# Kernel optimization log

Hardware: AMD Instinct MI355X
Metric: run time of the kernel (lower is better)

Reference implementation:

```python
import jax, jax.numpy as jnp
import numpy as np
import math

B, S, I, C = 1, 256, 512, 256   # batch, msa rows, residues, c_s
H, D = 8, 32                     # num_heads, head_dim; total = H*D = 256
EPS = 1e-5


def setup_inputs() -> dict:
    key = jax.random.key(0)
    ks = jax.random.split(key, 10)
    s = 0.02
    return {
        "msa_representation": jax.random.normal(ks[0], (B, S, I, C), jnp.float32),
        "ln_gamma": jnp.ones((C,), jnp.float32),
        "ln_beta": jnp.zeros((C,), jnp.float32),
        # weights stored [in, out] (torch Linear applies x @ W.T; equivalent math)
        "Wq": jax.random.normal(ks[1], (C, H * D), jnp.float32) * s,
        "Wk": jax.random.normal(ks[2], (C, D), jnp.float32) * s,
        "Wv": jax.random.normal(ks[3], (C, D), jnp.float32) * s,
        "Wg": jax.random.normal(ks[4], (C, H * D), jnp.float32) * s,
        "bg": jnp.zeros((H * D,), jnp.float32),
        "Wo": jax.random.normal(ks[5], (H * D, C), jnp.float32) * s,
        "bo": jnp.zeros((C,), jnp.float32),
    }


def reference(msa_representation, ln_gamma, ln_beta, Wq, Wk, Wv, Wg, bg, Wo, bo):
    x = msa_representation
    mu = jnp.mean(x, axis=-1, keepdims=True)
    var = jnp.mean(jnp.square(x - mu), axis=-1, keepdims=True)
    x = (x - mu) * jax.lax.rsqrt(var + EPS) * ln_gamma + ln_beta  # [B,S,I,C]

    Q = (x @ Wq).reshape(B, S, I, H, D).mean(axis=1)              # [B,I,H,D]
    K = x @ Wk                                                    # [B,S,I,D] ('btid')
    V = x @ Wv                                                    # [B,S,I,D]
    G = jax.nn.sigmoid(x @ Wg + bg).reshape(B, S, I, H, D)        # [B,S,I,H,D]

    scores = jnp.einsum('bihd,btid->bhti', Q, K) / math.sqrt(D)   # [B,H,S,I]
    attn = jax.nn.softmax(scores, axis=-2)                        # softmax over rows t
    weighted = jnp.einsum('bhti,btid->bihd', attn, V)             # [B,I,H,D]

    values = (G * weighted[:, None]).reshape(B, S, I, H * D)
    return values @ Wo + bo                                       # [B,S,I,C]
```

## Files before the change

### kernel.cpp

```cpp
#include <hip/hip_runtime.h>
#include <hip/hip_bf16.h>

#define S_DIM 256
#define I_DIM 512
#define NROWS (S_DIM * I_DIM)

using bf16x8 = __attribute__((ext_vector_type(8))) short;
using f32x4  = __attribute__((ext_vector_type(4))) float;
typedef unsigned short ushort_t;

__device__ __forceinline__ unsigned short f2bf(float f) {
  unsigned int u = __builtin_bit_cast(unsigned int, f);
  u += 0x7fffu + ((u >> 16) & 1u);
  return (unsigned short)(u >> 16);
}
__device__ __forceinline__ float bf2f(unsigned short u) {
  unsigned int x = ((unsigned int)u) << 16;
  return __builtin_bit_cast(float, x);
}
__device__ __forceinline__ void gl_lds16(const void* g, void* l) {
  __builtin_amdgcn_global_load_lds(
      (const __attribute__((address_space(1))) void*)g,
      (__attribute__((address_space(3))) void*)l, 16, 0, 0);
}

__global__ __launch_bounds__(256) void prep_weights(
    const float* __restrict__ Wk, const float* __restrict__ Wv,
    const float* __restrict__ Wg, const float* __restrict__ Wo,
    ushort_t* __restrict__ WkvT, ushort_t* __restrict__ WgT,
    ushort_t* __restrict__ WoT) {
  int t = blockIdx.x * 256 + threadIdx.x;
  int n = t >> 8, c = t & 255;
  if (t < 64 * 256) {
    float v = (n < 32) ? Wk[c * 32 + n] : Wv[c * 32 + (n - 32)];
    WkvT[t] = f2bf(v);
  }
  WgT[t] = f2bf(Wg[c * 256 + n]);
  WoT[t] = f2bf(Wo[c * 256 + n]);
}

__global__ __launch_bounds__(256) void ln_kernel(
    const float* __restrict__ x, const float* __restrict__ gamma,
    const float* __restrict__ beta, ushort_t* __restrict__ xn,
    float* __restrict__ xpart) {
  __shared__ float sacc[4][256];
  int b = blockIdx.x;
  int i = b & (I_DIM - 1);
  int sq = b >> 9;
  int w = threadIdx.x >> 6;
  int lane = threadIdx.x & 63;

  float4 gv = *(const float4*)(gamma + lane * 4);
  float4 bv = *(const float4*)(beta + lane * 4);
  float p0 = 0.f, p1 = 0.f, p2 = 0.f, p3 = 0.f;

#pragma unroll 4
  for (int it = 0; it < 16; ++it) {
    int s = sq * 64 + w * 16 + it;
    size_t row = (size_t)s * I_DIM + i;
    float4 xv = *(const float4*)(x + row * 256 + lane * 4);
    float sum = xv.x + xv.y + xv.z + xv.w;
    float sq2 = xv.x*xv.x + xv.y*xv.y + xv.z*xv.z + xv.w*xv.w;
#pragma unroll
    for (int off = 32; off >= 1; off >>= 1) {
      sum += __shfl_xor(sum, off);
      sq2 += __shfl_xor(sq2, off);
    }
    float mu = sum * (1.f / 256.f);
    float rs = rsqrtf(sq2 * (1.f / 256.f) - mu * mu + 1e-5f);
    float y0 = (xv.x - mu) * rs * gv.x + bv.x;
    float y1 = (xv.y - mu) * rs * gv.y + bv.y;
    float y2 = (xv.z - mu) * rs * gv.z + bv.z;
    float y3 = (xv.w - mu) * rs * gv.w + bv.w;
    ushort4 o;
    o.x = f2bf(y0); o.y = f2bf(y1); o.z = f2bf(y2); o.w = f2bf(y3);
    *(ushort4*)(xn + row * 256 + lane * 4) = o;
    p0 += y0; p1 += y1; p2 += y2; p3 += y3;
  }
  sacc[w][lane * 4 + 0] = p0;
  sacc[w][lane * 4 + 1] = p1;
  sacc[w][lane * 4 + 2] = p2;
  sacc[w][lane * 4 + 3] = p3;
  __syncthreads();
  int tid = threadIdx.x;
  xpart[((size_t)sq * I_DIM + i) * 256 + tid] =
      sacc[0][tid] + sacc[1][tid] + sacc[2][tid] + sacc[3][tid];
}

__global__ __launch_bounds__(256) void q_kernel(
    const float* __restrict__ xpart, const float* __restrict__ Wq,
    float* __restrict__ Q) {
  int i = blockIdx.x, col = threadIdx.x;
  __shared__ float xr[256];
  float s = xpart[((size_t)0 * I_DIM + i) * 256 + col]
          + xpart[((size_t)1 * I_DIM + i) * 256 + col]
          + xpart[((size_t)2 * I_DIM + i) * 256 + col]
          + xpart[((size_t)3 * I_DIM + i) * 256 + col];
  xr[col] = s * (1.f / 256.f);
  __syncthreads();
  float acc = 0.f;
#pragma unroll 8
  for (int c = 0; c < 256; ++c) acc = fmaf(xr[c], Wq[c * 256 + col], acc);
  Q[i * 256 + col] = acc * 0.17677669529663687f;
}

__global__ __launch_bounds__(256) void kv_kernel(
    const ushort_t* __restrict__ xn, const ushort_t* __restrict__ WkvT,
    ushort_t* __restrict__ KVb) {
  __shared__ __attribute__((aligned(16))) ushort_t xs[64 * 264];
  __shared__ __attribute__((aligned(16))) ushort_t wt[64 * 264];
  int tid = threadIdx.x;
  int m0 = blockIdx.x * 64;

  const uint4* xg = (const uint4*)(xn + (size_t)m0 * 256);
#pragma unroll
  for (int j = 0; j < 8; ++j) {
    int idx = tid + j * 256;
    *(uint4*)(&xs[(idx >> 5) * 264 + (idx & 31) * 8]) = xg[idx];
  }
  const uint4* wg_ = (const uint4*)WkvT;
#pragma unroll
  for (int j = 0; j < 8; ++j) {
    int idx = tid + j * 256;
    *(uint4*)(&wt[(idx >> 5) * 264 + (idx & 31) * 8]) = wg_[idx];
  }
  __syncthreads();

  int w = tid >> 6, lane = tid & 63;
  int m15 = lane & 15, q = lane >> 4;
  f32x4 acc[4] = {};
#pragma unroll
  for (int k = 0; k < 8; ++k) {
    bf16x8 a = *(const bf16x8*)(&xs[(w * 16 + m15) * 264 + k * 32 + q * 8]);
#pragma unroll
    for (int nt = 0; nt < 4; ++nt) {
      bf16x8 bb = *(const bf16x8*)(&wt[(nt * 16 + m15) * 264 + k * 32 + q * 8]);
      acc[nt] = __builtin_amdgcn_mfma_f32_16x16x32_bf16(a, bb, acc[nt], 0, 0, 0);
    }
  }
#pragma unroll
  for (int nt = 0; nt < 4; ++nt)
#pragma unroll
    for (int r = 0; r < 4; ++r)
      KVb[(size_t)(m0 + w * 16 + q * 4 + r) * 64 + nt * 16 + m15] = f2bf(acc[nt][r]);
}

__global__ __launch_bounds__(256) void attn_kernel(
    const ushort_t* __restrict__ KVb, const float* __restrict__ Q,
    float* __restrict__ weighted) {
  __shared__ ushort_t Vs[256 * 36];
  __shared__ float sl[8 * 264];
  __shared__ float ql[256];
  int i = blockIdx.x, tid = threadIdx.x;

  ql[tid] = Q[i * 256 + tid];
  const uint4* src = (const uint4*)(KVb + ((size_t)tid * I_DIM + i) * 64);
  uint4 kr0 = src[0], kr1 = src[1], kr2 = src[2], kr3 = src[3];
#pragma unroll
  for (int j = 0; j < 4; ++j) {
    uint4 v = src[4 + j];
    *(ushort4*)(&Vs[tid * 36 + j * 8 + 0]) = *(ushort4*)&v.x;
    *(ushort4*)(&Vs[tid * 36 + j * 8 + 4]) = *(ushort4*)&v.z;
  }
  ushort_t ks[32];
  *(uint4*)&ks[0] = kr0; *(uint4*)&ks[8] = kr1;
  *(uint4*)&ks[16] = kr2; *(uint4*)&ks[24] = kr3;
  float kf[32];
#pragma unroll
  for (int d = 0; d < 32; ++d) kf[d] = bf2f(ks[d]);
  __syncthreads();

#pragma unroll
  for (int h = 0; h < 8; ++h) {
    float sc = 0.f;
#pragma unroll
    for (int d = 0; d < 32; ++d) sc = fmaf(kf[d], ql[h * 32 + d], sc);
    sl[h * 264 + tid] = sc;
  }
  __syncthreads();

  int w = tid >> 6, lane = tid & 63;
#pragma unroll
  for (int hh = 0; hh < 2; ++hh) {
    int h = w * 2 + hh;
    float v0 = sl[h * 264 + lane], v1 = sl[h * 264 + lane + 64];
    float v2 = sl[h * 264 + lane + 128], v3 = sl[h * 264 + lane + 192];
    float m = fmaxf(fmaxf(v0, v1), fmaxf(v2, v3));
#pragma unroll
    for (int off = 32; off >= 1; off >>= 1) m = fmaxf(m, __shfl_xor(m, off));
    float e0 = __expf(v0 - m), e1 = __expf(v1 - m);
    float e2 = __expf(v2 - m), e3 = __expf(v3 - m);
    float ssum = e0 + e1 + e2 + e3;
#pragma unroll
    for (int off = 32; off >= 1; off >>= 1) ssum += __shfl_xor(ssum, off);
    float inv = 1.f / ssum;
    sl[h * 264 + lane] = e0 * inv;
    sl[h * 264 + lane + 64] = e1 * inv;
    sl[h * 264 + lane + 128] = e2 * inv;
    sl[h * 264 + lane + 192] = e3 * inv;
  }
  __syncthreads();

  int h = tid >> 5, d = tid & 31;
  float acc = 0.f;
#pragma unroll 4
  for (int t = 0; t < 256; ++t)
    acc = fmaf(sl[h * 264 + t], bf2f(Vs[t * 36 + d]), acc);
  weighted[i * 256 + tid] = acc;
}

__global__ __launch_bounds__(512) void gate_val_kernel(
    ushort_t* xv,
    const ushort_t* __restrict__ WgT, const float* __restrict__ weighted,
    const float* __restrict__ bg) {
  __shared__ __attribute__((aligned(16))) ushort_t As[128 * 64];
  __shared__ __attribute__((aligned(16))) ushort_t Bs[256 * 64];
  const int tid = threadIdx.x;
  const int m0 = blockIdx.x * 128;
  const int w = tid >> 6, lane = tid & 63;
  const int m15 = lane & 15, q = lane >> 4;
  const int r2 = w >> 2, c4 = w & 3;

  f32x4 acc[4][4];
  const f32x4 zero = {0.f, 0.f, 0.f, 0.f};
#pragma unroll
  for (int t = 0; t < 4; ++t)
#pragma unroll
    for (int nt = 0; nt < 4; ++nt) acc[t][nt] = zero;

#pragma unroll 1
  for (int kc = 0; kc < 4; ++kc) {
    __syncthreads();
#pragma unroll
    for (int it = 0; it < 2; ++it) {
      int L = it * 512 + tid;
      int r = L >> 3, u = (L & 7) ^ (r & 7);
      gl_lds16(xv + (size_t)(m0 + r) * 256 + kc * 64 + u * 8,
               &As[(it * 512 + w * 64) * 8]);
    }
#pragma unroll
    for (int it = 0; it < 4; ++it) {
      int L = it * 512 + tid;
      int n = L >> 3, u = (L & 7) ^ (n & 7);
      gl_lds16(WgT + (size_t)n * 256 + kc * 64 + u * 8,
               &Bs[(it * 512 + w * 64) * 8]);
    }
    __syncthreads();
#pragma unroll
    for (int kk = 0; kk < 2; ++kk) {
      bf16x8 bf[4], af[4];
#pragma unroll
      for (int nt = 0; nt < 4; ++nt) {
        int n = c4 * 64 + nt * 16 + m15;
        bf[nt] = *(const bf16x8*)&Bs[n * 64 + (((kk * 4 + q) ^ (n & 7)) * 8)];
      }
#pragma unroll
      for (int t = 0; t < 4; ++t) {
        int m = r2 * 64 + t * 16 + m15;
        af[t] = *(const bf16x8*)&As[m * 64 + (((kk * 4 + q) ^ (m & 7)) * 8)];
      }
#pragma unroll
      for (int t = 0; t < 4; ++t)
#pragma unroll
        for (int nt = 0; nt < 4; ++nt)
          acc[t][nt] = __builtin_amdgcn_mfma_f32_16x16x32_bf16(af[t], bf[nt], acc[t][nt], 0, 0, 0);
    }
  }

#pragma unroll
  for (int nt = 0; nt < 4; ++nt) {
    int col = c4 * 64 + nt * 16 + m15;
    float bgi = bg[col];
#pragma unroll
    for (int t = 0; t < 4; ++t)
#pragma unroll
      for (int r = 0; r < 4; ++r) {
        int row = r2 * 64 + t * 16 + q * 4 + r;
        float pre = acc[t][nt][r] + bgi;
        float g = 1.f / (1.f + __expf(-pre));
        float vv = g * weighted[(size_t)((m0 + row) & (I_DIM - 1)) * 256 + col];
        xv[(size_t)(m0 + row) * 256 + col] = f2bf(vv);
      }
  }
}

__global__ __launch_bounds__(512) void out_kernel(
    const ushort_t* __restrict__ val, const ushort_t* __restrict__ WoT,
    const float* __restrict__ bo, float* __restrict__ out) {
  __shared__ __attribute__((aligned(16))) ushort_t As[128 * 64];
  __shared__ __attribute__((aligned(16))) ushort_t Bs[256 * 64];
  const int tid = threadIdx.x;
  const int m0 = blockIdx.x * 128;
  const int w = tid >> 6, lane = tid & 63;
  const int m15 = lane & 15, q = lane >> 4;
  const int r2 = w >> 2, c4 = w & 3;

  f32x4 acc[4][4];
  const f32x4 zero = {0.f, 0.f, 0.f, 0.f};
#pragma unroll
  for (int t = 0; t < 4; ++t)
#pragma unroll
    for (int nt = 0; nt < 4; ++nt) acc[t][nt] = zero;

#pragma unroll 1
  for (int kc = 0; kc < 4; ++kc) {
    __syncthreads();
#pragma unroll
    for (int it = 0; it < 2; ++it) {
      int L = it * 512 + tid;
      int r = L >> 3, u = (L & 7) ^ (r & 7);
      gl_lds16(val + (size_t)(m0 + r) * 256 + kc * 64 + u * 8,
               &As[(it * 512 + w * 64) * 8]);
    }
#pragma unroll
    for (int it = 0; it < 4; ++it) {
      int L = it * 512 + tid;
      int n = L >> 3, u = (L & 7) ^ (n & 7);
      gl_lds16(WoT + (size_t)n * 256 + kc * 64 + u * 8,
               &Bs[(it * 512 + w * 64) * 8]);
    }
    __syncthreads();
#pragma unroll
    for (int kk = 0; kk < 2; ++kk) {
      bf16x8 bf[4], af[4];
#pragma unroll
      for (int nt = 0; nt < 4; ++nt) {
        int n = c4 * 64 + nt * 16 + m15;
        bf[nt] = *(const bf16x8*)&Bs[n * 64 + (((kk * 4 + q) ^ (n & 7)) * 8)];
      }
#pragma unroll
      for (int t = 0; t < 4; ++t) {
        int m = r2 * 64 + t * 16 + m15;
        af[t] = *(const bf16x8*)&As[m * 64 + (((kk * 4 + q) ^ (m & 7)) * 8)];
      }
#pragma unroll
      for (int t = 0; t < 4; ++t)
#pragma unroll
        for (int nt = 0; nt < 4; ++nt)
          acc[t][nt] = __builtin_amdgcn_mfma_f32_16x16x32_bf16(af[t], bf[nt], acc[t][nt], 0, 0, 0);
    }
  }

#pragma unroll
  for (int nt = 0; nt < 4; ++nt) {
    int col = c4 * 64 + nt * 16 + m15;
    float boi = bo[col];
#pragma unroll
    for (int t = 0; t < 4; ++t)
#pragma unroll
      for (int r = 0; r < 4; ++r) {
        int row = r2 * 64 + t * 16 + q * 4 + r;
        out[(size_t)(m0 + row) * 256 + col] = acc[t][nt][r] + boi;
      }
  }
}

extern "C" void kernel_launch(void* const* d_in, const int* in_sizes, int n_in,
                              void* d_out, int out_size, void* d_ws, size_t ws_size,
                              hipStream_t stream) {
  const float* msa = (const float*)d_in[0];
  const float* gam = (const float*)d_in[1];
  const float* bet = (const float*)d_in[2];
  const float* Wq  = (const float*)d_in[3];
  const float* Wk  = (const float*)d_in[4];
  const float* Wv  = (const float*)d_in[5];
  const float* Wg  = (const float*)d_in[6];
  const float* bg  = (const float*)d_in[7];
  const float* Wo  = (const float*)d_in[8];
  const float* bo  = (const float*)d_in[9];
  float* out = (float*)d_out;

  char* ws = (char*)d_ws;
  ushort_t* xn     = (ushort_t*)ws;
  float* xpart     = (float*)(ws + 67108864);
  float* Q         = (float*)(ws + 69206016);
  ushort_t* KVb    = (ushort_t*)(ws + 69730304);
  float* weighted  = (float*)(ws + 86507520);
  ushort_t* WkvT   = (ushort_t*)(ws + 87031808);
  ushort_t* WgT    = (ushort_t*)(ws + 87064576);
  ushort_t* WoT    = (ushort_t*)(ws + 87195648);

  prep_weights<<<256, 256, 0, stream>>>(Wk, Wv, Wg, Wo, WkvT, WgT, WoT);
  ln_kernel<<<2048, 256, 0, stream>>>(msa, gam, bet, xn, xpart);
  q_kernel<<<512, 256, 0, stream>>>(xpart, Wq, Q);
  kv_kernel<<<2048, 256, 0, stream>>>(xn, WkvT, KVb);
  attn_kernel<<<512, 256, 0, stream>>>(KVb, Q, weighted);
  gate_val_kernel<<<1024, 512, 0, stream>>>(xn, WgT, weighted, bg);
  out_kernel<<<1024, 512, 0, stream>>>(xn, WoT, bo, out);
}
```

Measured before the change: 392.9 us.

## Make gate and output GEMMs persistent with register-resident weights and double-buffered rows

The gate and output GEMM kernels now run 256 blocks. Each block loads the full 256x256 bf16 weight matrix into LDS once, keeps each wave's 32-column weight slice in registers, and streams 512 rows in 32-row tiles through a double-buffered LDS area. This removes the repeated weight reloads and per-k-chunk synchronisation of the earlier 128-row tiling, and the epilogues now use vectorized float4/ushort4 stores. In exchange it uses about 160KB of LDS per block, allowing one block per CU, and the tiles are small, so latency hiding depends on the prefetch overlap.

```diff
diff --git a/kernel.cpp b/kernel.cpp
--- a/kernel.cpp
+++ b/kernel.cpp
@@ -213,145 +213,178 @@
     ushort_t* xv,
     const ushort_t* __restrict__ WgT, const float* __restrict__ weighted,
     const float* __restrict__ bg) {
-  __shared__ __attribute__((aligned(16))) ushort_t As[128 * 64];
-  __shared__ __attribute__((aligned(16))) ushort_t Bs[256 * 64];
+  __shared__ __attribute__((aligned(16))) ushort_t Wl[256 * 256];
+  __shared__ __attribute__((aligned(16))) ushort_t Ab[2][32 * 256];
   const int tid = threadIdx.x;
-  const int m0 = blockIdx.x * 128;
   const int w = tid >> 6, lane = tid & 63;
   const int m15 = lane & 15, q = lane >> 4;
-  const int r2 = w >> 2, c4 = w & 3;
-
-  f32x4 acc[4][4];
-  const f32x4 zero = {0.f, 0.f, 0.f, 0.f};
-#pragma unroll
-  for (int t = 0; t < 4; ++t)
-#pragma unroll
-    for (int nt = 0; nt < 4; ++nt) acc[t][nt] = zero;
+  const size_t base = (size_t)blockIdx.x * 512;
+
+#pragma unroll
+  for (int it = 0; it < 16; ++it) {
+    int L = it * 512 + tid;
+    int n = L >> 5, u = L & 31;
+    int us = (u & 24) | ((u & 7) ^ (n & 7));
+    gl_lds16(WgT + (size_t)n * 256 + us * 8, &Wl[(it * 512 + w * 64) * 8]);
+  }
+#pragma unroll
+  for (int it = 0; it < 2; ++it) {
+    int L = it * 512 + tid;
+    int r = L >> 5, u = L & 31;
+    int us = (u & 24) | ((u & 7) ^ (r & 7));
+    gl_lds16(xv + (base + r) * 256 + us * 8, &Ab[0][(it * 512 + w * 64) * 8]);
+  }
+  __syncthreads();
+
+  bf16x8 wgf[2][8];
+#pragma unroll
+  for (int ct = 0; ct < 2; ++ct) {
+    int n = w * 32 + ct * 16 + m15;
+#pragma unroll
+    for (int kk = 0; kk < 8; ++kk) {
+      int ku = kk * 4 + q;
+      int us = (ku & 24) | ((ku & 7) ^ (n & 7));
+      wgf[ct][kk] = *(const bf16x8*)&Wl[n * 256 + us * 8];
+    }
+  }
 
 #pragma unroll 1
-  for (int kc = 0; kc < 4; ++kc) {
+  for (int t = 0; t < 16; ++t) {
+    const int cur = t & 1;
+    if (t < 15) {
+#pragma unroll
+      for (int it = 0; it < 2; ++it) {
+        int L = it * 512 + tid;
+        int r = L >> 5, u = L & 31;
+        int us = (u & 24) | ((u & 7) ^ (r & 7));
+        gl_lds16(xv + (base + (size_t)(t + 1) * 32 + r) * 256 + us * 8,
+                 &Ab[cur ^ 1][(it * 512 + w * 64) * 8]);
+      }
+    }
+    f32x4 acc[2][2];
+    const f32x4 zero = {0.f, 0.f, 0.f, 0.f};
+    acc[0][0] = zero; acc[0][1] = zero; acc[1][0] = zero; acc[1][1] = zero;
+#pragma unroll
+    for (int kk = 0; kk < 8; ++kk) {
+      int ku = kk * 4 + q;
+      int ub = (ku & 24) | ((ku & 7) ^ (m15 & 7));
+      bf16x8 b0 = *(const bf16x8*)&Ab[cur][(0 * 16 + m15) * 256 + ub * 8];
+      bf16x8 b1 = *(const bf16x8*)&Ab[cur][(1 * 16 + m15) * 256 + ub * 8];
+#pragma unroll
+      for (int ct = 0; ct < 2; ++ct) {
+        acc[ct][0] = __builtin_amdgcn_mfma_f32_16x16x32_bf16(wgf[ct][kk], b0, acc[ct][0], 0, 0, 0);
+        acc[ct][1] = __builtin_amdgcn_mfma_f32_16x16x32_bf16(wgf[ct][kk], b1, acc[ct][1], 0, 0, 0);
+      }
+    }
+#pragma unroll
+    for (int mt = 0; mt < 2; ++mt) {
+      size_t row = base + (size_t)t * 32 + mt * 16 + m15;
+      int i = (int)(row & (I_DIM - 1));
+#pragma unroll
+      for (int ct = 0; ct < 2; ++ct) {
+        int col0 = w * 32 + ct * 16 + q * 4;
+        float4 wv = *(const float4*)(weighted + (size_t)i * 256 + col0);
+        float4 bgv = *(const float4*)(bg + col0);
+        float p0 = acc[ct][mt][0] + bgv.x;
+        float p1 = acc[ct][mt][1] + bgv.y;
+        float p2 = acc[ct][mt][2] + bgv.z;
+        float p3 = acc[ct][mt][3] + bgv.w;
+        float g0 = 1.f / (1.f + __expf(-p0));
+        float g1 = 1.f / (1.f + __expf(-p1));
+        float g2 = 1.f / (1.f + __expf(-p2));
+        float g3 = 1.f / (1.f + __expf(-p3));
+        ushort4 o;
+        o.x = f2bf(g0 * wv.x); o.y = f2bf(g1 * wv.y);
+        o.z = f2bf(g2 * wv.z); o.w = f2bf(g3 * wv.w);
+        *(ushort4*)(xv + row * 256 + col0) = o;
+      }
+    }
     __syncthreads();
-#pragma unroll
-    for (int it = 0; it < 2; ++it) {
-      int L = it * 512 + tid;
-      int r = L >> 3, u = (L & 7) ^ (r & 7);
-      gl_lds16(xv + (size_t)(m0 + r) * 256 + kc * 64 + u * 8,
-               &As[(it * 512 + w * 64) * 8]);
-    }
-#pragma unroll
-    for (int it = 0; it < 4; ++it) {
-      int L = it * 512 + tid;
-      int n = L >> 3, u = (L & 7) ^ (n & 7);
-      gl_lds16(WgT + (size_t)n * 256 + kc * 64 + u * 8,
-               &Bs[(it * 512 + w * 64) * 8]);
-    }
-    __syncthreads();
-#pragma unroll
-    for (int kk = 0; kk < 2; ++kk) {
-      bf16x8 bf[4], af[4];
-#pragma unroll
-      for (int nt = 0; nt < 4; ++nt) {
-        int n = c4 * 64 + nt * 16 + m15;
-        bf[nt] = *(const bf16x8*)&Bs[n * 64 + (((kk * 4 + q) ^ (n & 7)) * 8)];
-      }
-#pragma unroll
-      for (int t = 0; t < 4; ++t) {
-        int m = r2 * 64 + t * 16 + m15;
-        af[t] = *(const bf16x8*)&As[m * 64 + (((kk * 4 + q) ^ (m & 7)) * 8)];
-      }
-#pragma unroll
-      for (int t = 0; t < 4; ++t)
-#pragma unroll
-        for (int nt = 0; nt < 4; ++nt)
-          acc[t][nt] = __builtin_amdgcn_mfma_f32_16x16x32_bf16(af[t], bf[nt], acc[t][nt], 0, 0, 0);
-    }
-  }
-
-#pragma unroll
-  for (int nt = 0; nt < 4; ++nt) {
-    int col = c4 * 64 + nt * 16 + m15;
-    float bgi = bg[col];
-#pragma unroll
-    for (int t = 0; t < 4; ++t)
-#pragma unroll
-      for (int r = 0; r < 4; ++r) {
-        int row = r2 * 64 + t * 16 + q * 4 + r;
-        float pre = acc[t][nt][r] + bgi;
-        float g = 1.f / (1.f + __expf(-pre));
-        float vv = g * weighted[(size_t)((m0 + row) & (I_DIM - 1)) * 256 + col];
-        xv[(size_t)(m0 + row) * 256 + col] = f2bf(vv);
-      }
   }
 }
 
 __global__ __launch_bounds__(512) void out_kernel(
     const ushort_t* __restrict__ val, const ushort_t* __restrict__ WoT,
     const float* __restrict__ bo, float* __restrict__ out) {
-  __shared__ __attribute__((aligned(16))) ushort_t As[128 * 64];
-  __shared__ __attribute__((aligned(16))) ushort_t Bs[256 * 64];
+  __shared__ __attribute__((aligned(16))) ushort_t Wl[256 * 256];
+  __shared__ __attribute__((aligned(16))) ushort_t Ab[2][32 * 256];
   const int tid = threadIdx.x;
-  const int m0 = blockIdx.x * 128;
   const int w = tid >> 6, lane = tid & 63;
   const int m15 = lane & 15, q = lane >> 4;
-  const int r2 = w >> 2, c4 = w & 3;
-
-  f32x4 acc[4][4];
-  const f32x4 zero = {0.f, 0.f, 0.f, 0.f};
-#pragma unroll
-  for (int t = 0; t < 4; ++t)
-#pragma unroll
-    for (int nt = 0; nt < 4; ++nt) acc[t][nt] = zero;
+  const size_t base = (size_t)blockIdx.x * 512;
+
+#pragma unroll
+  for (int it = 0; it < 16; ++it) {
+    int L = it * 512 + tid;
+    int n = L >> 5, u = L & 31;
+    int us = (u & 24) | ((u & 7) ^ (n & 7));
+    gl_lds16(WoT + (size_t)n * 256 + us * 8, &Wl[(it * 512 + w * 64) * 8]);
+  }
+#pragma unroll
+  for (int it = 0; it < 2; ++it) {
+    int L = it * 512 + tid;
+    int r = L >> 5, u = L & 31;
+    int us = (u & 24) | ((u & 7) ^ (r & 7));
+    gl_lds16(val + (base + r) * 256 + us * 8, &Ab[0][(it * 512 + w * 64) * 8]);
+  }
+  __syncthreads();
+
+  bf16x8 wof[2][8];
+#pragma unroll
+  for (int ct = 0; ct < 2; ++ct) {
+    int n = w * 32 + ct * 16 + m15;
+#pragma unroll
+    for (int kk = 0; kk < 8; ++kk) {
+      int ku = kk * 4 + q;
+      int us = (ku & 24) | ((ku & 7) ^ (n & 7));
+      wof[ct][kk] = *(const bf16x8*)&Wl[n * 256 + us * 8];
+    }
+  }
 
 #pragma unroll 1
-  for (int kc = 0; kc < 4; ++kc) {
+  for (int t = 0; t < 16; ++t) {
+    const int cur = t & 1;
+    if (t < 15) {
+#pragma unroll
+      for (int it = 0; it < 2; ++it) {
+        int L = it * 512 + tid;
+        int r = L >> 5, u = L & 31;
+        int us = (u & 24) | ((u & 7) ^ (r & 7));
+        gl_lds16(val + (base + (size_t)(t + 1) * 32 + r) * 256 + us * 8,
+                 &Ab[cur ^ 1][(it * 512 + w * 64) * 8]);
+      }
+    }
+    f32x4 acc[2][2];
+    const f32x4 zero = {0.f, 0.f, 0.f, 0.f};
+    acc[0][0] = zero; acc[0][1] = zero; acc[1][0] = zero; acc[1][1] = zero;
+#pragma unroll
+    for (int kk = 0; kk < 8; ++kk) {
+      int ku = kk * 4 + q;
+      int ub = (ku & 24) | ((ku & 7) ^ (m15 & 7));
+      bf16x8 b0 = *(const bf16x8*)&Ab[cur][(0 * 16 + m15) * 256 + ub * 8];
+      bf16x8 b1 = *(const bf16x8*)&Ab[cur][(1 * 16 + m15) * 256 + ub * 8];
+#pragma unroll
+      for (int ct = 0; ct < 2; ++ct) {
+        acc[ct][0] = __builtin_amdgcn_mfma_f32_16x16x32_bf16(wof[ct][kk], b0, acc[ct][0], 0, 0, 0);
+        acc[ct][1] = __builtin_amdgcn_mfma_f32_16x16x32_bf16(wof[ct][kk], b1, acc[ct][1], 0, 0, 0);
+      }
+    }
+#pragma unroll
+    for (int mt = 0; mt < 2; ++mt) {
+      size_t row = base + (size_t)t * 32 + mt * 16 + m15;
+#pragma unroll
+      for (int ct = 0; ct < 2; ++ct) {
+        int col0 = w * 32 + ct * 16 + q * 4;
+        float4 bov = *(const float4*)(bo + col0);
+        float4 ov;
+        ov.x = acc[ct][mt][0] + bov.x;
+        ov.y = acc[ct][mt][1] + bov.y;
+        ov.z = acc[ct][mt][2] + bov.z;
+        ov.w = acc[ct][mt][3] + bov.w;
+        *(float4*)(out + row * 256 + col0) = ov;
+      }
+    }
     __syncthreads();
-#pragma unroll
-    for (int it = 0; it < 2; ++it) {
-      int L = it * 512 + tid;
-      int r = L >> 3, u = (L & 7) ^ (r & 7);
-      gl_lds16(val + (size_t)(m0 + r) * 256 + kc * 64 + u * 8,
-               &As[(it * 512 + w * 64) * 8]);
-    }
-#pragma unroll
-    for (int it = 0; it < 4; ++it) {
-      int L = it * 512 + tid;
-      int n = L >> 3, u = (L & 7) ^ (n & 7);
-      gl_lds16(WoT + (size_t)n * 256 + kc * 64 + u * 8,
-               &Bs[(it * 512 + w * 64) * 8]);
-    }
-    __syncthreads();
-#pragma unroll
-    for (int kk = 0; kk < 2; ++kk) {
-      bf16x8 bf[4], af[4];
-#pragma unroll
-      for (int nt = 0; nt < 4; ++nt) {
-        int n = c4 * 64 + nt * 16 + m15;
-        bf[nt] = *(const bf16x8*)&Bs[n * 64 + (((kk * 4 + q) ^ (n & 7)) * 8)];
-      }
-#pragma unroll
-      for (int t = 0; t < 4; ++t) {
-        int m = r2 * 64 + t * 16 + m15;
-        af[t] = *(const bf16x8*)&As[m * 64 + (((kk * 4 + q) ^ (m & 7)) * 8)];
-      }
-#pragma unroll
-      for (int t = 0; t < 4; ++t)
-#pragma unroll
-        for (int nt = 0; nt < 4; ++nt)
-          acc[t][nt] = __builtin_amdgcn_mfma_f32_16x16x32_bf16(af[t], bf[nt], acc[t][nt], 0, 0, 0);
-    }
-  }
-
-#pragma unroll
-  for (int nt = 0; nt < 4; ++nt) {
-    int col = c4 * 64 + nt * 16 + m15;
-    float boi = bo[col];
-#pragma unroll
-    for (int t = 0; t < 4; ++t)
-#pragma unroll
-      for (int r = 0; r < 4; ++r) {
-        int row = r2 * 64 + t * 16 + q * 4 + r;
-        out[(size_t)(m0 + row) * 256 + col] = acc[t][nt][r] + boi;
-      }
   }
 }
 
@@ -385,6 +418,6 @@
   q_kernel<<<512, 256, 0, stream>>>(xpart, Wq, Q);
   kv_kernel<<<2048, 256, 0, stream>>>(xn, WkvT, KVb);
   attn_kernel<<<512, 256, 0, stream>>>(KVb, Q, weighted);
-  gate_val_kernel<<<1024, 512, 0, stream>>>(xn, WgT, weighted, bg);
-  out_kernel<<<1024, 512, 0, stream>>>(xn, WoT, bo, out);
-}
+  gate_val_kernel<<<256, 512, 0, stream>>>(xn, WgT, weighted, bg);
+  out_kernel<<<256, 512, 0, stream>>>(xn, WoT, bo, out);
+}
```

Measured after the change: 371.7 us. 5.4% less time.
